# Kernel tuning notes

Measured on AMD Instinct MI355X. Metric: run time of the kernel, lower is better.

Reference implementation:

```python
import jax, jax.numpy as jnp
import numpy as np

N_NODES = 50000
N_EDGES = 800000
NUM_GRAPHS = 64
NEG_SLOPE = 0.2


def gatv2_layer(x, src, dst, Wl, bl, Wr, br, att, b_out, heads, out_ch, concat):
    # PyG GATv2Conv: x_j = lin_l(x)[src], x_i = lin_r(x)[dst]
    N = x.shape[0]
    xl = (x @ Wl + bl).reshape(N, heads, out_ch)
    xr = (x @ Wr + br).reshape(N, heads, out_ch)
    m = xl[src] + xr[dst]                                  # [E, H, C]
    e = jax.nn.leaky_relu(m, negative_slope=NEG_SLOPE)
    logits = jnp.einsum('ehc,hc->eh', e, att)              # [E, H]
    # softmax over incoming edges of each destination node
    seg_max = jax.ops.segment_max(logits, dst, num_segments=N)
    ex = jnp.exp(logits - seg_max[dst])
    denom = jax.ops.segment_sum(ex, dst, num_segments=N)
    alpha = ex / denom[dst]                                # [E, H]
    out = jax.ops.segment_sum(alpha[..., None] * xl[src], dst, num_segments=N)
    out = out.reshape(N, heads * out_ch) if concat else out.mean(axis=1)
    return out + b_out


def _forward(x, edge_index, batch,
             Wl1, bl1, Wr1, br1, att1, b1,
             Wl2, bl2, Wr2, br2, att2, b2,
             Wl3, bl3, Wr3, br3, att3, b3,
             Wm1, bm1, Wm2, bm2):
    N = x.shape[0]
    loops = jnp.arange(N, dtype=edge_index.dtype)
    src = jnp.concatenate([edge_index[0], loops])          # add_self_loops=True
    dst = jnp.concatenate([edge_index[1], loops])
    h = jax.nn.relu(gatv2_layer(x, src, dst, Wl1, bl1, Wr1, br1, att1, b1, 4, 64, True))
    h = jax.nn.relu(gatv2_layer(h, src, dst, Wl2, bl2, Wr2, br2, att2, b2, 2, 64, True))
    h = jax.nn.relu(gatv2_layer(h, src, dst, Wl3, bl3, Wr3, br3, att3, b3, 1, 64, False))
    # global_mean_pool
    sums = jax.ops.segment_sum(h, batch, num_segments=NUM_GRAPHS)
    counts = jax.ops.segment_sum(jnp.ones((N, 1), h.dtype), batch, num_segments=NUM_GRAPHS)
    pooled = sums / jnp.maximum(counts, 1.0)
    return jax.nn.relu(pooled @ Wm1 + bm1) @ Wm2 + bm2


def setup_inputs() -> dict:
    key = jax.random.key(0)
    ks = jax.random.split(key, 24)
    s = 0.05
    inp = {
        'x': jax.random.normal(ks[0], (N_NODES, 128), jnp.float32),
        'edge_index': jax.random.randint(ks[1], (2, N_EDGES), 0, N_NODES, jnp.int64),
        'batch': jnp.sort(jax.random.randint(ks[2], (N_NODES,), 0, NUM_GRAPHS, jnp.int64)),
        # conv1: in=128, heads=4, C=64
        'Wl1': jax.random.normal(ks[3], (128, 256), jnp.float32) * s,
        'bl1': jnp.zeros((256,), jnp.float32),
        'Wr1': jax.random.normal(ks[4], (128, 256), jnp.float32) * s,
        'br1': jnp.zeros((256,), jnp.float32),
        'att1': jax.random.normal(ks[5], (4, 64), jnp.float32) * s,
        'b1': jnp.zeros((256,), jnp.float32),
        # conv2: in=256, heads=2, C=64
        'Wl2': jax.random.normal(ks[6], (256, 128), jnp.float32) * s,
        'bl2': jnp.zeros((128,), jnp.float32),
        'Wr2': jax.random.normal(ks[7], (256, 128), jnp.float32) * s,
        'br2': jnp.zeros((128,), jnp.float32),
        'att2': jax.random.normal(ks[8], (2, 64), jnp.float32) * s,
        'b2': jnp.zeros((128,), jnp.float32),
        # conv3: in=128, heads=1, C=64, concat=False
        'Wl3': jax.random.normal(ks[9], (128, 64), jnp.float32) * s,
        'bl3': jnp.zeros((64,), jnp.float32),
        'Wr3': jax.random.normal(ks[10], (128, 64), jnp.float32) * s,
        'br3': jnp.zeros((64,), jnp.float32),
        'att3': jax.random.normal(ks[11], (1, 64), jnp.float32) * s,
        'b3': jnp.zeros((64,), jnp.float32),
        # MLP 64 -> 32 -> 2
        'Wm1': jax.random.normal(ks[12], (64, 32), jnp.float32) * s,
        'bm1': jnp.zeros((32,), jnp.float32),
        'Wm2': jax.random.normal(ks[13], (32, 2), jnp.float32) * s,
        'bm2': jnp.zeros((2,), jnp.float32),
    }
    return inp


def reference(x, edge_index, batch,
              Wl1, bl1, Wr1, br1, att1, b1,
              Wl2, bl2, Wr2, br2, att2, b2,
              Wl3, bl3, Wr3, br3, att3, b3,
              Wm1, bm1, Wm2, bm2):
    return _forward(x, edge_index, batch,
                    Wl1, bl1, Wr1, br1, att1, b1,
                    Wl2, bl2, Wr2, br2, att2, b2,
                    Wl3, bl3, Wr3, br3, att3, b3,
                    Wm1, bm1, Wm2, bm2)
```

## Files before the change

### kernel.cpp

```cpp
#include <hip/hip_runtime.h>


typedef _Float16 half_t;
typedef _Float16 h2    __attribute__((ext_vector_type(2)));
typedef _Float16 f16x8 __attribute__((ext_vector_type(8)));
typedef float    f32x4 __attribute__((ext_vector_type(4)));

#define SORT_BLOCKS 64
#define SCAN_BLOCKS 256

#if __has_builtin(__builtin_amdgcn_fdot2)
#define FDOT2(a, b, c) __builtin_amdgcn_fdot2((a), (b), (c), false)
#else
#define FDOT2(a, b, c) ((c) + (float)(a)[0] * (float)(b)[0] + (float)(a)[1] * (float)(b)[1])
#endif

__global__ void cvt_kernel(const float* __restrict__ in,
                           half_t* __restrict__ out, int n)
{
    int i = (blockIdx.x * blockDim.x + threadIdx.x) * 4;
    if (i >= n) return;
    float4 v = *reinterpret_cast<const float4*>(in + i);
    half_t o[4] = {(half_t)v.x, (half_t)v.y, (half_t)v.z, (half_t)v.w};
    *reinterpret_cast<uint2*>(out + i) = *reinterpret_cast<const uint2*>(o);
}

__global__ void cvt_wt_all_kernel(
    const float* __restrict__ Wl1, const float* __restrict__ Wr1, half_t* __restrict__ T1l, half_t* __restrict__ T1r,
    const float* __restrict__ Wl2, const float* __restrict__ Wr2, half_t* __restrict__ T2l, half_t* __restrict__ T2r,
    const float* __restrict__ Wl3, const float* __restrict__ Wr3, half_t* __restrict__ T3l, half_t* __restrict__ T3r)
{
    int id = blockIdx.x * blockDim.x + threadIdx.x;
    const float* W; half_t* T; int K, No, idx;
    if (id < 2 * 32768) {
        K = 128; No = 256; idx = id & 32767;
        W = (id < 32768) ? Wl1 : Wr1; T = (id < 32768) ? T1l : T1r;
    } else if (id < 2 * 32768 + 2 * 32768) {
        int v = id - 65536; K = 256; No = 128; idx = v & 32767;
        W = (v < 32768) ? Wl2 : Wr2; T = (v < 32768) ? T2l : T2r;
    } else {
        int v = id - 131072; if (v >= 2 * 8192) return;
        K = 128; No = 64; idx = v & 8191;
        W = (v < 8192) ? Wl3 : Wr3; T = (v < 8192) ? T3l : T3r;
    }
    int n = idx / K, k = idx - n * K;
    T[idx] = (half_t)W[(size_t)k * No + n];
}

template <int K, int NY>
__global__ __launch_bounds__(256) void gemm_slab(
    const half_t* __restrict__ A,
    const half_t* __restrict__ W0, const half_t* __restrict__ W1,
    const float* __restrict__ bias0, const float* __restrict__ bias1,
    half_t* __restrict__ OutL, half_t* __restrict__ OutR,
    int M)
{
    constexpr int CPR = K / 8;
    __shared__ __align__(16) char As[64 * K * 2];
    __shared__ __align__(16) char Bs[64 * 128 * 2];

    const int t = threadIdx.x;
    const int lane = t & 63;
    const int wid = t >> 6;
    const int row0 = blockIdx.x * 64;

    #pragma unroll
    for (int i = 0; i < (64 * CPR) / 256; ++i) {
        int c16 = i * 256 + t;
        int r = c16 / CPR, j = c16 % CPR;
        int gr = row0 + r; if (gr > M - 1) gr = M - 1;
        uint4 v = *reinterpret_cast<const uint4*>(A + (size_t)gr * K + j * 8);
        *reinterpret_cast<uint4*>(As + r * (2 * K) + ((j ^ (r & 7)) << 4)) = v;
    }

    const int ra = wid * 16 + (lane & 15);
    const int rowA_byte = ra * (2 * K);

    for (int z = 0; z < 2; ++z) {
        const half_t* Wt = z ? W1 : W0;
        const float* bias = z ? bias1 : bias0;
        half_t* Out = z ? OutR : OutL;
        for (int y = 0; y < NY; ++y) {
            f32x4 acc[4];
            #pragma unroll
            for (int j = 0; j < 4; ++j) acc[j] = (f32x4){0.f, 0.f, 0.f, 0.f};

            #pragma unroll
            for (int kh = 0; kh < K / 128; ++kh) {
                __syncthreads();
                #pragma unroll
                for (int i = 0; i < 4; ++i) {
                    int c16 = i * 256 + t;
                    int n = c16 >> 4, j = c16 & 15;
                    uint4 v = *reinterpret_cast<const uint4*>(
                        Wt + (size_t)(y * 64 + n) * K + kh * 128 + j * 8);
                    *reinterpret_cast<uint4*>(Bs + n * 256 + ((j ^ (n & 7)) << 4)) = v;
                }
                __syncthreads();
                #pragma unroll
                for (int ks = 0; ks < 4; ++ks) {
                    int chA = kh * 16 + ks * 4 + (lane >> 4);
                    f16x8 a = *reinterpret_cast<const f16x8*>(
                        As + rowA_byte + ((chA ^ (ra & 7)) << 4));
                    #pragma unroll
                    for (int j = 0; j < 4; ++j) {
                        int nb = j * 16 + (lane & 15);
                        int chB = ks * 4 + (lane >> 4);
                        f16x8 b = *reinterpret_cast<const f16x8*>(
                            Bs + nb * 256 + ((chB ^ (nb & 7)) << 4));
                        acc[j] = __builtin_amdgcn_mfma_f32_16x16x32_f16(a, b, acc[j], 0, 0, 0);
                    }
                }
            }
            __syncthreads();
            #pragma unroll
            for (int j = 0; j < 4; ++j) {
                float bb = bias[y * 64 + j * 16 + (lane & 15)];
                #pragma unroll
                for (int q = 0; q < 4; ++q) {
                    int r = wid * 16 + (lane >> 4) * 4 + q;
                    int c = j * 16 + (lane & 15);
                    *reinterpret_cast<half_t*>(Bs + r * 128 + c * 2)
                        = (half_t)(acc[j][q] + bb);
                }
            }
            __syncthreads();
            {
                int r = t >> 2, ch = t & 3;
                int gr = row0 + r;
                if (gr < M) {
                    const uint4* src = reinterpret_cast<const uint4*>(Bs + r * 128 + ch * 32);
                    uint4 v0 = src[0], v1 = src[1];
                    uint4* dst = reinterpret_cast<uint4*>(
                        Out + ((size_t)y * M + gr) * 64 + ch * 16);
                    dst[0] = v0; dst[1] = v1;
                }
            }
        }
    }
}

__global__ void hist_kernel(const int* __restrict__ ei, int E, int Etot,
                            int* __restrict__ deg)
{
    int i = blockIdx.x * blockDim.x + threadIdx.x;
    if (i >= Etot) return;
    int d = (i < E) ? ei[E + i] : (i - E);
    atomicAdd(&deg[d], 1);
}

__global__ __launch_bounds__(256) void scan1_kernel(
    const int* __restrict__ deg, int* __restrict__ blockSums, int N)
{
    __shared__ int red[256];
    const int b = blockIdx.x, t = threadIdx.x;
    const int chunk = (N + SCAN_BLOCKS - 1) / SCAN_BLOCKS;
    const int lo = b * chunk;
    const int hi = (lo + chunk < N) ? lo + chunk : N;
    int s = 0;
    for (int i = lo + t; i < hi; i += 256) s += deg[i];
    red[t] = s;
    __syncthreads();
    #pragma unroll
    for (int off = 128; off > 0; off >>= 1) {
        if (t < off) red[t] += red[t + off];
        __syncthreads();
    }
    if (t == 0) blockSums[b] = red[0];
}

__global__ __launch_bounds__(256) void scan2_kernel(
    const int* __restrict__ blockSums, int* __restrict__ blockBase,
    int* __restrict__ rowptr, int N)
{
    __shared__ int tmp[256];
    const int t = threadIdx.x;
    int v = blockSums[t];
    tmp[t] = v;
    __syncthreads();
    for (int off = 1; off < 256; off <<= 1) {
        int u = (t >= off) ? tmp[t - off] : 0;
        __syncthreads();
        tmp[t] += u;
        __syncthreads();
    }
    blockBase[t] = tmp[t] - v;
    if (t == 255) rowptr[N] = tmp[255];
}

__global__ __launch_bounds__(256) void scan3_kernel(
    const int* __restrict__ deg, const int* __restrict__ blockBase,
    int* __restrict__ rowptr, int* __restrict__ cursor, int N)
{
    __shared__ int tmp[256];
    __shared__ int carry;
    const int b = blockIdx.x, t = threadIdx.x;
    const int chunk = (N + SCAN_BLOCKS - 1) / SCAN_BLOCKS;
    const int lo = b * chunk;
    const int hi = (lo + chunk < N) ? lo + chunk : N;
    if (t == 0) carry = blockBase[b];
    __syncthreads();
    for (int j = lo; j < hi; j += 256) {
        int i = j + t;
        int v = (i < hi) ? deg[i] : 0;
        tmp[t] = v;
        __syncthreads();
        for (int off = 1; off < 256; off <<= 1) {
            int u = (t >= off) ? tmp[t - off] : 0;
            __syncthreads();
            tmp[t] += u;
            __syncthreads();
        }
        int excl = carry + tmp[t] - v;
        if (i < hi) { rowptr[i] = excl; cursor[i] = excl; }
        __syncthreads();
        if (t == 255) carry += tmp[255];
        __syncthreads();
    }
}

__global__ void scatter_kernel(const int* __restrict__ ei, int E, int Etot,
                               int* __restrict__ cursor, int* __restrict__ ssrc)
{
    int i = blockIdx.x * blockDim.x + threadIdx.x;
    if (i >= Etot) return;
    int d, s;
    if (i < E) { s = ei[i]; d = ei[E + i]; }
    else       { s = i - E; d = s; }
    int pos = atomicAdd(&cursor[d], 1);
    ssrc[pos] = s;
}

__global__ __launch_bounds__(256) void dhist2_kernel(
    const int* __restrict__ rowptr, int* __restrict__ blockHist, int N)
{
    __shared__ int lh[256];
    lh[threadIdx.x] = 0;
    __syncthreads();
    const int chunk = (N + SORT_BLOCKS - 1) / SORT_BLOCKS;
    const int lo = blockIdx.x * chunk;
    const int hi = (lo + chunk < N) ? lo + chunk : N;
    for (int d = lo + threadIdx.x; d < hi; d += 256) {
        int deg = rowptr[d + 1] - rowptr[d];
        atomicAdd(&lh[deg > 255 ? 255 : deg], 1);
    }
    __syncthreads();
    blockHist[blockIdx.x * 256 + threadIdx.x] = lh[threadIdx.x];
}

__global__ __launch_bounds__(256) void dscan2_kernel(
    const int* __restrict__ blockHist, int* __restrict__ blockOff)
{
    const int t = threadIdx.x;
    int total = 0;
    for (int b = 0; b < SORT_BLOCKS; ++b) total += blockHist[b * 256 + t];
    __shared__ int tmp[256];
    tmp[t] = total;
    __syncthreads();
    for (int off = 1; off < 256; off <<= 1) {
        int v = (t >= off) ? tmp[t - off] : 0;
        __syncthreads();
        tmp[t] += v;
        __syncthreads();
    }
    int grand = tmp[255];
    int start = grand - tmp[t];
    for (int b = 0; b < SORT_BLOCKS; ++b) {
        blockOff[b * 256 + t] = start;
        start += blockHist[b * 256 + t];
    }
}

__global__ __launch_bounds__(256) void dscatter2_kernel(
    const int* __restrict__ rowptr, const int* __restrict__ blockOff,
    int* __restrict__ dperm, int N)
{
    __shared__ int cur[256];
    cur[threadIdx.x] = blockOff[blockIdx.x * 256 + threadIdx.x];
    __syncthreads();
    const int chunk = (N + SORT_BLOCKS - 1) / SORT_BLOCKS;
    const int lo = blockIdx.x * chunk;
    const int hi = (lo + chunk < N) ? lo + chunk : N;
    for (int d = lo + threadIdx.x; d < hi; d += 256) {
        int deg = rowptr[d + 1] - rowptr[d];
        int pos = atomicAdd(&cur[deg > 255 ? 255 : deg], 1);
        dperm[pos] = d;
    }
}

template <int H, bool OUT_F32, bool OUT_F16>
__global__ __launch_bounds__(256) void gat_fused4(
    const int* __restrict__ rowptr, const int* __restrict__ ssrc,
    const int* __restrict__ dperm,
    const half_t* __restrict__ xl, const half_t* __restrict__ xr,
    const float* __restrict__ att, const float* __restrict__ bias,
    float* __restrict__ outf, half_t* __restrict__ outb, int N)
{
    const int gid = blockIdx.x * 64 + (threadIdx.x >> 2);
    const int sub = threadIdx.x & 3;
    if (gid >= N * H) return;
    const int h  = gid / N;
    const int di = gid - h * N;
    const int d  = dperm[di];
    const int HC = H * 64;
    const int so = sub * 16;

    const half_t* xlh = xl + (size_t)h * N * 64;
    const h2 c02 = {(half_t)0.2f, (half_t)0.2f};

    h2 xrv[8], attv[8], acc[8];
    {
        const half_t* pr = xr + ((size_t)h * N + d) * 64 + so;
        uint4 rb[2];
        rb[0] = *reinterpret_cast<const uint4*>(pr);
        rb[1] = *reinterpret_cast<const uint4*>(pr + 8);
        const h2* rp = reinterpret_cast<const h2*>(rb);
        const float* pa = att + h * 64 + so;
        #pragma unroll
        for (int k = 0; k < 8; ++k) {
            xrv[k] = rp[k];
            attv[k] = (h2){(half_t)pa[2 * k], (half_t)pa[2 * k + 1]};
            acc[k] = (h2){(half_t)0.f, (half_t)0.f};
        }
    }
    float M = -3.0e38f, S = 0.f;

    const int begin = rowptr[d], end = rowptr[d + 1];
    uint4 cbuf[2], b1[2];
    {
        const half_t* pl = xlh + (size_t)ssrc[begin] * 64 + so;
        cbuf[0] = *reinterpret_cast<const uint4*>(pl);
        cbuf[1] = *reinterpret_cast<const uint4*>(pl + 8);
    }
    if (begin + 1 < end) {
        const half_t* pl = xlh + (size_t)ssrc[begin + 1] * 64 + so;
        b1[0] = *reinterpret_cast<const uint4*>(pl);
        b1[1] = *reinterpret_cast<const uint4*>(pl + 8);
    }
    for (int e = begin; e < end; ++e) {
        uint4 b2[2];
        const bool have2 = (e + 2 < end);
        if (have2) {
            const half_t* pl = xlh + (size_t)ssrc[e + 2] * 64 + so;
            b2[0] = *reinterpret_cast<const uint4*>(pl);
            b2[1] = *reinterpret_cast<const uint4*>(pl + 8);
        }
        const h2* cur = reinterpret_cast<const h2*>(cbuf);
        float p = 0.f;
        #pragma unroll
        for (int k = 0; k < 8; ++k) {
            h2 m = cur[k] + xrv[k];
            h2 v = __builtin_elementwise_max(m, m * c02);
            p = FDOT2(v, attv[k], p);
        }
        p += __shfl_xor(p, 1);
        p += __shfl_xor(p, 2);
        float nM = fmaxf(M, p);
        float scale = __expf(M - nM);
        float w = __expf(p - nM);
        S = fmaf(S, scale, w);
        h2 s2 = {(half_t)scale, (half_t)scale};
        h2 w2 = {(half_t)w, (half_t)w};
        #pragma unroll
        for (int k = 0; k < 8; ++k) acc[k] = acc[k] * s2 + cur[k] * w2;
        M = nM;
        if (e + 1 < end) { cbuf[0] = b1[0]; cbuf[1] = b1[1]; }
        if (have2)       { b1[0] = b2[0]; b1[1] = b2[1]; }
    }
    float inv = 1.f / S;
    const float* pb = bias + h * 64 + so;
    float res[16];
    #pragma unroll
    for (int k = 0; k < 8; ++k) {
        float v0 = fmaf((float)acc[k][0], inv, pb[2 * k]);
        float v1 = fmaf((float)acc[k][1], inv, pb[2 * k + 1]);
        res[2 * k]     = v0 > 0.f ? v0 : 0.f;
        res[2 * k + 1] = v1 > 0.f ? v1 : 0.f;
    }
    size_t ob = (size_t)d * HC + h * 64 + so;
    if (OUT_F32) {
        #pragma unroll
        for (int k = 0; k < 16; k += 4) {
            float4 v = {res[k], res[k+1], res[k+2], res[k+3]};
            *reinterpret_cast<float4*>(outf + ob + k) = v;
        }
    }
    if (OUT_F16) {
        half_t o[16];
        #pragma unroll
        for (int k = 0; k < 16; ++k) o[k] = (half_t)res[k];
        const uint4* ov = reinterpret_cast<const uint4*>(o);
        *reinterpret_cast<uint4*>(outb + ob) = ov[0];
        *reinterpret_cast<uint4*>(outb + ob + 8) = ov[1];
    }
}

__global__ __launch_bounds__(256) void pool_kernel2(
    const float* __restrict__ h3, const int* __restrict__ batch,
    float* __restrict__ sums, float* __restrict__ counts, int N)
{
    const int wave = blockIdx.x * 4 + (threadIdx.x >> 6);
    const int lane = threadIdx.x & 63;
    const int n0 = wave * 64;
    if (n0 >= N) return;
    const int n1 = (n0 + 64 < N) ? n0 + 64 : N;
    float s = 0.f, cnt = 0.f;
    int g = batch[n0];
    for (int n = n0; n < n1; ++n) {
        int gn = batch[n];
        if (gn != g) {
            atomicAdd(&sums[g * 64 + lane], s);
            if (lane == 0) atomicAdd(&counts[g], cnt);
            s = 0.f; cnt = 0.f; g = gn;
        }
        s += h3[(size_t)n * 64 + lane];
        cnt += 1.f;
    }
    atomicAdd(&sums[g * 64 + lane], s);
    if (lane == 0) atomicAdd(&counts[g], cnt);
}

__global__ __launch_bounds__(64) void mlp_kernel(
    const float* __restrict__ sums, const float* __restrict__ counts,
    const float* __restrict__ Wm1, const float* __restrict__ bm1,
    const float* __restrict__ Wm2, const float* __restrict__ bm2,
    float* __restrict__ out)
{
    int g = blockIdx.x;
    int t = threadIdx.x;
    __shared__ float pooled[64];
    __shared__ float hidden[32];
    float cnt = counts[g];
    cnt = cnt > 1.f ? cnt : 1.f;
    pooled[t] = sums[g * 64 + t] / cnt;
    __syncthreads();
    if (t < 32) {
        float a = bm1[t];
        #pragma unroll
        for (int k = 0; k < 64; ++k) a = fmaf(pooled[k], Wm1[k * 32 + t], a);
        hidden[t] = a > 0.f ? a : 0.f;
    }
    __syncthreads();
    if (t < 2) {
        float a = bm2[t];
        #pragma unroll
        for (int j = 0; j < 32; ++j) a = fmaf(hidden[j], Wm2[j * 2 + t], a);
        out[g * 2 + t] = a;
    }
}

static void run_layer(const half_t* Xb, int K, int H,
                      const float* bl, const float* br,
                      const float* att, const float* bias_out,
                      const half_t* Wtl, const half_t* Wtr,
                      const int* rowptr, const int* ssrc, const int* dperm, int N,
                      half_t* xl, half_t* xr,
                      float* houtf, half_t* houtb,
                      hipStream_t stream)
{
    int gblocks = (N + 63) / 64;
    if (K == 128 && H == 4)
        gemm_slab<128, 4><<<gblocks, 256, 0, stream>>>(Xb, Wtl, Wtr, bl, br, xl, xr, N);
    else if (K == 256)
        gemm_slab<256, 2><<<gblocks, 256, 0, stream>>>(Xb, Wtl, Wtr, bl, br, xl, xr, N);
    else
        gemm_slab<128, 1><<<gblocks, 256, 0, stream>>>(Xb, Wtl, Wtr, bl, br, xl, xr, N);

    int ngroups = N * H;
    int blocks = (ngroups + 63) / 64;
    if (H == 4)
        gat_fused4<4, false, true><<<blocks, 256, 0, stream>>>(
            rowptr, ssrc, dperm, xl, xr, att, bias_out, houtf, houtb, N);
    else if (H == 2)
        gat_fused4<2, false, true><<<blocks, 256, 0, stream>>>(
            rowptr, ssrc, dperm, xl, xr, att, bias_out, houtf, houtb, N);
    else
        gat_fused4<1, true, false><<<blocks, 256, 0, stream>>>(
            rowptr, ssrc, dperm, xl, xr, att, bias_out, houtf, houtb, N);
}

extern "C" void kernel_launch(void* const* d_in, const int* in_sizes, int n_in,
                              void* d_out, int out_size, void* d_ws, size_t ws_size,
                              hipStream_t stream)
{
    const float* x    = (const float*)d_in[0];
    const int*   ei   = (const int*)d_in[1];
    const int*   batch= (const int*)d_in[2];
    const float* Wl1 = (const float*)d_in[3];
    const float* bl1 = (const float*)d_in[4];
    const float* Wr1 = (const float*)d_in[5];
    const float* br1 = (const float*)d_in[6];
    const float* att1= (const float*)d_in[7];
    const float* b1  = (const float*)d_in[8];
    const float* Wl2 = (const float*)d_in[9];
    const float* bl2 = (const float*)d_in[10];
    const float* Wr2 = (const float*)d_in[11];
    const float* br2 = (const float*)d_in[12];
    const float* att2= (const float*)d_in[13];
    const float* b2  = (const float*)d_in[14];
    const float* Wl3 = (const float*)d_in[15];
    const float* bl3 = (const float*)d_in[16];
    const float* Wr3 = (const float*)d_in[17];
    const float* br3 = (const float*)d_in[18];
    const float* att3= (const float*)d_in[19];
    const float* b3  = (const float*)d_in[20];
    const float* Wm1 = (const float*)d_in[21];
    const float* bm1 = (const float*)d_in[22];
    const float* Wm2 = (const float*)d_in[23];
    const float* bm2 = (const float*)d_in[24];

    const int N    = in_sizes[2];
    const int E    = in_sizes[1] / 2;
    const int Etot = E + N;
    const int K1   = in_sizes[0] / N;

    char* wsb = (char*)d_ws;
    size_t o = 0;
    auto alloc = [&](size_t bytes) { char* p = wsb + o; o += (bytes + 255) & ~(size_t)255; return p; };
    half_t* xl    = (half_t*)alloc((size_t)N * 256 * 2);
    half_t* xr    = (half_t*)alloc((size_t)N * 256 * 2);
    half_t* xb    = (half_t*)alloc((size_t)N * K1 * 2);
    half_t* h1b   = (half_t*)alloc((size_t)N * 256 * 2);
    half_t* h2b   = (half_t*)alloc((size_t)N * 128 * 2);
    float*  h3f   = (float*)alloc((size_t)N * 64 * 4);
    int*   deg    = (int*)alloc((size_t)N * 4);
    int*   rowptr = (int*)alloc((size_t)(N + 1) * 4);
    int*   cursor = (int*)alloc((size_t)N * 4);
    int*   ssrc   = (int*)alloc((size_t)Etot * 4);
    int*   dperm  = (int*)alloc((size_t)N * 4);
    int*   blockHist = (int*)alloc((size_t)SORT_BLOCKS * 256 * 4);
    int*   blockOff  = (int*)alloc((size_t)SORT_BLOCKS * 256 * 4);
    int*   blockSums = (int*)alloc((size_t)SCAN_BLOCKS * 4);
    int*   blockBase = (int*)alloc((size_t)SCAN_BLOCKS * 4);
    half_t* Wt1l = (half_t*)alloc(128 * 256 * 2);
    half_t* Wt1r = (half_t*)alloc(128 * 256 * 2);
    half_t* Wt2l = (half_t*)alloc(256 * 128 * 2);
    half_t* Wt2r = (half_t*)alloc(256 * 128 * 2);
    half_t* Wt3l = (half_t*)alloc(128 * 64 * 2);
    half_t* Wt3r = (half_t*)alloc(128 * 64 * 2);
    float* sums   = (float*)alloc(64 * 64 * 4);
    float* counts = (float*)alloc(64 * 4);
    (void)ws_size; (void)n_in; (void)out_size;

    hipMemsetAsync(deg, 0, (size_t)N * 4, stream);
    hist_kernel<<<(Etot + 255) / 256, 256, 0, stream>>>(ei, E, Etot, deg);
    scan1_kernel<<<SCAN_BLOCKS, 256, 0, stream>>>(deg, blockSums, N);
    scan2_kernel<<<1, 256, 0, stream>>>(blockSums, blockBase, rowptr, N);
    scan3_kernel<<<SCAN_BLOCKS, 256, 0, stream>>>(deg, blockBase, rowptr, cursor, N);
    scatter_kernel<<<(Etot + 255) / 256, 256, 0, stream>>>(ei, E, Etot, cursor, ssrc);
    dhist2_kernel<<<SORT_BLOCKS, 256, 0, stream>>>(rowptr, blockHist, N);
    dscan2_kernel<<<1, 256, 0, stream>>>(blockHist, blockOff);
    dscatter2_kernel<<<SORT_BLOCKS, 256, 0, stream>>>(rowptr, blockOff, dperm, N);

    cvt_kernel<<<((N * K1) / 4 + 255) / 256, 256, 0, stream>>>(x, xb, N * K1);
    cvt_wt_all_kernel<<<(147456 + 255) / 256, 256, 0, stream>>>(
        Wl1, Wr1, Wt1l, Wt1r, Wl2, Wr2, Wt2l, Wt2r, Wl3, Wr3, Wt3l, Wt3r);

    run_layer(xb, K1, 4, bl1, br1, att1, b1, Wt1l, Wt1r,
              rowptr, ssrc, dperm, N, xl, xr, nullptr, h1b, stream);
    run_layer(h1b, 256, 2, bl2, br2, att2, b2, Wt2l, Wt2r,
              rowptr, ssrc, dperm, N, xl, xr, nullptr, h2b, stream);
    run_layer(h2b, 128, 1, bl3, br3, att3, b3, Wt3l, Wt3r,
              rowptr, ssrc, dperm, N, xl, xr, h3f, nullptr, stream);

    hipMemsetAsync(sums, 0, 64 * 64 * 4, stream);
    hipMemsetAsync(counts, 0, 64 * 4, stream);
    {
        int waves = (N + 63) / 64;
        pool_kernel2<<<(waves + 3) / 4, 256, 0, stream>>>(h3f, batch, sums, counts, N);
    }
    mlp_kernel<<<64, 64, 0, stream>>>(sums, counts, Wm1, bm1, Wm2, bm2, (float*)d_out);
}
```

Before: 371.8 us.

## Pre-bucket edges by source before CSR scatter to order neighbor lists

Adds a first counting-sort pass that buckets edges by source node, then scatters them into destination-major CSR from that source-ordered list. Within each destination's neighbor list the sources come out roughly ascending, which is meant to improve locality of the xl[src] gathers in the three attention layers. The cost is an extra histogram, scan and scatter pass plus two Etot-sized temporary arrays. Atomic cursor ordering is still nondeterministic, so the ordering is only approximate.

```diff
diff --git a/kernel.cpp b/kernel.cpp
--- a/kernel.cpp
+++ b/kernel.cpp
@@ -149,8 +149,17 @@
     atomicAdd(&deg[d], 1);
 }
 
+__global__ void shist_kernel(const int* __restrict__ ei, int E, int Etot,
+                             int* __restrict__ sdeg)
+{
+    int i = blockIdx.x * blockDim.x + threadIdx.x;
+    if (i >= Etot) return;
+    int s = (i < E) ? ei[i] : (i - E);
+    atomicAdd(&sdeg[s], 1);
+}
+
 __global__ __launch_bounds__(256) void scan1_kernel(
-    const int* __restrict__ deg, int* __restrict__ blockSums, int N)
+    const int* __restrict__ vals, int* __restrict__ blockSums, int N)
 {
     __shared__ int red[256];
     const int b = blockIdx.x, t = threadIdx.x;
@@ -158,7 +167,7 @@
     const int lo = b * chunk;
     const int hi = (lo + chunk < N) ? lo + chunk : N;
     int s = 0;
-    for (int i = lo + t; i < hi; i += 256) s += deg[i];
+    for (int i = lo + t; i < hi; i += 256) s += vals[i];
     red[t] = s;
     __syncthreads();
     #pragma unroll
@@ -171,7 +180,7 @@
 
 __global__ __launch_bounds__(256) void scan2_kernel(
     const int* __restrict__ blockSums, int* __restrict__ blockBase,
-    int* __restrict__ rowptr, int N)
+    int* __restrict__ outptr, int N)
 {
     __shared__ int tmp[256];
     const int t = threadIdx.x;
@@ -185,12 +194,12 @@
         __syncthreads();
     }
     blockBase[t] = tmp[t] - v;
-    if (t == 255) rowptr[N] = tmp[255];
+    if (t == 255) outptr[N] = tmp[255];
 }
 
 __global__ __launch_bounds__(256) void scan3_kernel(
-    const int* __restrict__ deg, const int* __restrict__ blockBase,
-    int* __restrict__ rowptr, int* __restrict__ cursor, int N)
+    const int* __restrict__ vals, const int* __restrict__ blockBase,
+    int* __restrict__ outptr, int* __restrict__ outcur, int N)
 {
     __shared__ int tmp[256];
     __shared__ int carry;
@@ -202,7 +211,7 @@
     __syncthreads();
     for (int j = lo; j < hi; j += 256) {
         int i = j + t;
-        int v = (i < hi) ? deg[i] : 0;
+        int v = (i < hi) ? vals[i] : 0;
         tmp[t] = v;
         __syncthreads();
         for (int off = 1; off < 256; off <<= 1) {
@@ -212,23 +221,34 @@
             __syncthreads();
         }
         int excl = carry + tmp[t] - v;
-        if (i < hi) { rowptr[i] = excl; cursor[i] = excl; }
+        if (i < hi) { outptr[i] = excl; outcur[i] = excl; }
         __syncthreads();
         if (t == 255) carry += tmp[255];
         __syncthreads();
     }
 }
 
-__global__ void scatter_kernel(const int* __restrict__ ei, int E, int Etot,
-                               int* __restrict__ cursor, int* __restrict__ ssrc)
+__global__ void sscatter_kernel(const int* __restrict__ ei, int E, int Etot,
+                                int* __restrict__ scursor,
+                                int* __restrict__ ses, int* __restrict__ sed)
 {
     int i = blockIdx.x * blockDim.x + threadIdx.x;
     if (i >= Etot) return;
-    int d, s;
+    int s, d;
     if (i < E) { s = ei[i]; d = ei[E + i]; }
     else       { s = i - E; d = s; }
-    int pos = atomicAdd(&cursor[d], 1);
-    ssrc[pos] = s;
+    int pos = atomicAdd(&scursor[s], 1);
+    ses[pos] = s; sed[pos] = d;
+}
+
+__global__ void scatter2_kernel(const int* __restrict__ ses,
+                                const int* __restrict__ sed, int Etot,
+                                int* __restrict__ cursor, int* __restrict__ ssrc)
+{
+    int i = blockIdx.x * blockDim.x + threadIdx.x;
+    if (i >= Etot) return;
+    int pos = atomicAdd(&cursor[sed[i]], 1);
+    ssrc[pos] = ses[i];
 }
 
 __global__ __launch_bounds__(256) void dhist2_kernel(
@@ -524,9 +544,14 @@
     half_t* h2b   = (half_t*)alloc((size_t)N * 128 * 2);
     float*  h3f   = (float*)alloc((size_t)N * 64 * 4);
     int*   deg    = (int*)alloc((size_t)N * 4);
+    int*   sdeg   = (int*)alloc((size_t)N * 4);
     int*   rowptr = (int*)alloc((size_t)(N + 1) * 4);
     int*   cursor = (int*)alloc((size_t)N * 4);
+    int*   srowptr= (int*)alloc((size_t)(N + 1) * 4);
+    int*   scursor= (int*)alloc((size_t)N * 4);
     int*   ssrc   = (int*)alloc((size_t)Etot * 4);
+    int*   ses    = (int*)alloc((size_t)Etot * 4);
+    int*   sed    = (int*)alloc((size_t)Etot * 4);
     int*   dperm  = (int*)alloc((size_t)N * 4);
     int*   blockHist = (int*)alloc((size_t)SORT_BLOCKS * 256 * 4);
     int*   blockOff  = (int*)alloc((size_t)SORT_BLOCKS * 256 * 4);
@@ -543,11 +568,17 @@
     (void)ws_size; (void)n_in; (void)out_size;
 
     hipMemsetAsync(deg, 0, (size_t)N * 4, stream);
+    hipMemsetAsync(sdeg, 0, (size_t)N * 4, stream);
     hist_kernel<<<(Etot + 255) / 256, 256, 0, stream>>>(ei, E, Etot, deg);
+    shist_kernel<<<(Etot + 255) / 256, 256, 0, stream>>>(ei, E, Etot, sdeg);
     scan1_kernel<<<SCAN_BLOCKS, 256, 0, stream>>>(deg, blockSums, N);
     scan2_kernel<<<1, 256, 0, stream>>>(blockSums, blockBase, rowptr, N);
     scan3_kernel<<<SCAN_BLOCKS, 256, 0, stream>>>(deg, blockBase, rowptr, cursor, N);
-    scatter_kernel<<<(Etot + 255) / 256, 256, 0, stream>>>(ei, E, Etot, cursor, ssrc);
+    scan1_kernel<<<SCAN_BLOCKS, 256, 0, stream>>>(sdeg, blockSums, N);
+    scan2_kernel<<<1, 256, 0, stream>>>(blockSums, blockBase, srowptr, N);
+    scan3_kernel<<<SCAN_BLOCKS, 256, 0, stream>>>(sdeg, blockBase, srowptr, scursor, N);
+    sscatter_kernel<<<(Etot + 255) / 256, 256, 0, stream>>>(ei, E, Etot, scursor, ses, sed);
+    scatter2_kernel<<<(Etot + 255) / 256, 256, 0, stream>>>(ses, sed, Etot, cursor, ssrc);
     dhist2_kernel<<<SORT_BLOCKS, 256, 0, stream>>>(rowptr, blockHist, N);
     dscan2_kernel<<<1, 256, 0, stream>>>(blockHist, blockOff);
     dscatter2_kernel<<<SORT_BLOCKS, 256, 0, stream>>>(rowptr, blockOff, dperm, N);
```

Result: slower. 446.5 us (+20.1%).
